# Kernel tuning notes

Measured on AMD Instinct MI355X. Metric: run time of the kernel, lower is better.

## Reference

```python
import jax, jax.numpy as jnp
import numpy as np

B, T, NB, D, E = 2, 4096, 4, 512, 4096
TEMP = 1.0
CAP_F = 1.5
NOISE_KEY = 42


def setup_inputs() -> dict:
    key = jax.random.key(0)
    k1, k2 = jax.random.split(key)
    x = jax.random.normal(k1, (B, T, NB * D), dtype=jnp.float32)
    # Tied weights: embedding_table[i].weight is embedding_decoder[i].weight, shape [E, D] per block
    W = jax.random.normal(k2, (NB, E, D), dtype=jnp.float32) * 0.02
    return {"x": x, "W": W}


def reference(x, W):
    Bv, Tv, _ = x.shape
    xb = x.reshape(Bv, Tv, NB, D)
    expert_capacity = int(Bv * Tv / E * CAP_F)  # = 3 here
    # per-block decoder logits: [B, T, NB, E]
    dist_logits = jnp.einsum('btnd,ned->btne', xb, W)
    # noise = 1 - temperature * rand_like(logits)
    noise = 1.0 - TEMP * jax.random.uniform(jax.random.key(NOISE_KEY), dist_logits.shape, dtype=dist_logits.dtype)
    noisy = dist_logits * noise
    # top-k over the token axis T (dim=1 in torch) per (b, block, element)
    nt = noisy.transpose(0, 2, 3, 1)  # [B, NB, E, T]
    _, topk_idx = jax.lax.top_k(nt, expert_capacity)  # [B, NB, E, k]
    mask = jnp.zeros(nt.shape, dtype=bool)
    bI = jnp.arange(Bv)[:, None, None, None]
    nI = jnp.arange(NB)[None, :, None, None]
    eI = jnp.arange(E)[None, None, :, None]
    mask = mask.at[bI, nI, eI, topk_idx].set(True)
    maskf = mask.transpose(0, 3, 1, 2).astype(noisy.dtype)  # [B, T, NB, E]
    # argmax over codebook dim of masked noisy logits
    decoded_indices = jnp.argmax(maskf * noisy, axis=-1)  # [B, T, NB]
    # embedding gather with tied table W[n]: [B, T, NB, D]
    latents = jax.vmap(lambda w, i: w[i], in_axes=(0, 2), out_axes=2)(W, decoded_indices)
    decoded_latents = latents.reshape(Bv, Tv, NB * D)  # cat along dim=2
    return decoded_indices, decoded_latents, dist_logits
```

## Files before the change

kernel.cpp:

```cpp
#include <hip/hip_runtime.h>
#include <stdint.h>

#define B_     2
#define T_     4096
#define NB_    4
#define D_     512
#define E_     4096
#define NE_    16384
#define HALF_  67108864u
#define SLOTS_ 32768
#define XN8_   2097152
#define WN8_   1048576
#define MT_    32
#define RECN_  (64 * NE_)

typedef unsigned long long u64;
typedef uint32_t u32;
typedef uint16_t u16;
typedef _Float16 f16x8 __attribute__((ext_vector_type(8)));
typedef float    f32x4 __attribute__((ext_vector_type(4)));

#define GLD(srcp, dstp) __builtin_amdgcn_global_load_lds( \
    (const __attribute__((address_space(1))) void*)(srcp), \
    (__attribute__((address_space(3))) void*)(dstp), 16, 0, 0)

__device__ __forceinline__ u32 rotl32(u32 x, int r) { return __builtin_rotateleft32(x, r); }

__device__ __forceinline__ void tf_0_42(u32 x0, u32 x1, u32 &o0, u32 &o1) {
  const u32 ks0 = 0u, ks1 = 42u, ks2 = 0x1BD11BDAu ^ 0u ^ 42u;
  x0 += ks0; x1 += ks1;
#define TFR(r) { x0 += x1; x1 = rotl32(x1, (r)); x1 ^= x0; }
  TFR(13) TFR(15) TFR(26) TFR(6)
  x0 += ks1; x1 += ks2 + 1u;
  TFR(17) TFR(29) TFR(16) TFR(24)
  x0 += ks2; x1 += ks0 + 2u;
  TFR(13) TFR(15) TFR(26) TFR(6)
  x0 += ks0; x1 += ks1 + 3u;
  TFR(17) TFR(29) TFR(16) TFR(24)
  x0 += ks1; x1 += ks2 + 4u;
  TFR(13) TFR(15) TFR(26) TFR(6)
  x0 += ks2; x1 += ks0 + 5u;
#undef TFR
  o0 = x0; o1 = x1;
}

__device__ __forceinline__ float noise_at(u32 i) {
  u32 o0, o1; tf_0_42(0u, i, o0, o1);
  u32 bits = o0 ^ o1;
  float f = __uint_as_float((bits >> 9) | 0x3F800000u);
  return 2.0f - f;
}

__device__ __forceinline__ u32 map_f32(float v) {
  u32 u = __float_as_uint(v);
  u32 s = (u32)((int)u >> 31);
  return u ^ (s | 0x80000000u);
}

__device__ __forceinline__ void merge3(u64 &a0, u64 &a1, u64 &a2,
                                       u64 b0, u64 b1, u64 b2) {
  u64 o0, o1, o2;
  if (a0 >= b0) {
    o0 = a0;
    if (a1 >= b0) { o1 = a1; o2 = (a2 >= b0) ? a2 : b0; }
    else          { o1 = b0; o2 = (a1 >= b1) ? a1 : b1; }
  } else {
    o0 = b0;
    if (b1 >= a0) { o1 = b1; o2 = (b2 >= a0) ? b2 : a0; }
    else          { o1 = a0; o2 = (b1 >= a1) ? b1 : a1; }
  }
  a0 = o0; a1 = o1; a2 = o2;
}

#define BASE_KEY 0x80000000FFFFFFFFull
#define SCALE_   2048.0f
#define INV_SC   (1.0f / 4194304.0f)

__global__ __launch_bounds__(256) void init_keys(u64* __restrict__ keys,
                                                 u32* __restrict__ thr) {
  int i = blockIdx.x * 256 + threadIdx.x;
  keys[i] = BASE_KEY;
  thr[i]  = 0u;
}

__device__ __forceinline__ void split8v(const float4 a0, const float4 a1, f16x8 &hi, f16x8 &lo) {
  float fv[8] = {a0.x, a0.y, a0.z, a0.w, a1.x, a1.y, a1.z, a1.w};
#pragma unroll
  for (int j = 0; j < 8; ++j) {
    float f = fv[j] * SCALE_;
    _Float16 h = (_Float16)f;
    hi[j] = h;
    lo[j] = (_Float16)(f - (float)h);
  }
}

__global__ __launch_bounds__(256) void presplit(const float* __restrict__ x,
                                                const float* __restrict__ W,
                                                f16x8* __restrict__ xh, f16x8* __restrict__ xl,
                                                f16x8* __restrict__ wh, f16x8* __restrict__ wl) {
  size_t g = (size_t)blockIdx.x * 256 + threadIdx.x;
  const float4* src;
  f16x8 *dh, *dl;
  size_t off;
  if (g < XN8_) { src = (const float4*)x; dh = xh; dl = xl; off = g; }
  else          { src = (const float4*)W; dh = wh; dl = wl; off = g - XN8_; }
  float4 a0 = src[off * 2], a1 = src[off * 2 + 1];
  f16x8 hi, lo;
  split8v(a0, a1, hi, lo);
  dh[off] = hi; dl[off] = lo;
}

#define BM 128
#define BN 128

__device__ __forceinline__ void stage_tile(const f16x8* __restrict__ xh,
                                           const f16x8* __restrict__ xl,
                                           const f16x8* __restrict__ wh,
                                           const f16x8* __restrict__ wl,
                                           f16x8* buf, int m0, int n, int e0,
                                           int k0, int w, int lane) {
#pragma unroll
  for (int i = 0; i < 2; ++i) {
    int sbase = w * 128 + i * 64;
    int s  = sbase + lane;
    int r  = s >> 2;
    int ko = (s & 3) ^ ((r >> 1) & 3);
    size_t gA = ((size_t)(m0 + r) * NB_ + n) * (D_ / 8) + k0 + ko;
    size_t gB = ((size_t)n * E_ + e0 + r) * (D_ / 8) + k0 + ko;
    GLD(xh + gA, buf + sbase);
    GLD(xl + gA, buf + 512 + sbase);
    GLD(wh + gB, buf + 1024 + sbase);
    GLD(wl + gB, buf + 1536 + sbase);
  }
}

__device__ __forceinline__ void compute_step(const f16x8* buf, f32x4 acc[4][4],
                                             int wr, int wc, int lm, int lk) {
  const f16x8* Ah = buf;
  const f16x8* Al = buf + 512;
  const f16x8* Bh = buf + 1024;
  const f16x8* Bl = buf + 1536;
  f16x8 bh[4], bl[4];
#pragma unroll
  for (int fn = 0; fn < 4; ++fn) {
    int row = wc * 64 + fn * 16 + lm;
    int ps  = lk ^ ((row >> 1) & 3);
    bh[fn] = Bh[row * 4 + ps];
    bl[fn] = Bl[row * 4 + ps];
  }
#pragma unroll
  for (int fm = 0; fm < 4; ++fm) {
    int row = wr * 64 + fm * 16 + lm;
    int ps  = lk ^ ((row >> 1) & 3);
    f16x8 ah = Ah[row * 4 + ps];
    f16x8 al = Al[row * 4 + ps];
#pragma unroll
    for (int fn = 0; fn < 4; ++fn) {
      acc[fm][fn] = __builtin_amdgcn_mfma_f32_16x16x32_f16(ah, bh[fn], acc[fm][fn], 0, 0, 0);
      acc[fm][fn] = __builtin_amdgcn_mfma_f32_16x16x32_f16(ah, bl[fn], acc[fm][fn], 0, 0, 0);
      acc[fm][fn] = __builtin_amdgcn_mfma_f32_16x16x32_f16(al, bh[fn], acc[fm][fn], 0, 0, 0);
    }
  }
}

__global__ __launch_bounds__(256) void gemm_presample(const f16x8* __restrict__ xh,
                                                      const f16x8* __restrict__ xl,
                                                      const f16x8* __restrict__ wh,
                                                      const f16x8* __restrict__ wl,
                                                      u32* __restrict__ thrbuf) {
  __shared__ f16x8 lds_raw[2048];
  f16x8* AhV = lds_raw;
  f16x8* AlV = lds_raw + 512;
  f16x8* BhV = lds_raw + 1024;
  f16x8* BlV = lds_raw + 1536;

  const int id = blockIdx.x;
  const int e0 = (id & 31) * BN;
  const int n  = (id >> 5) & 3;
  const int b  = id >> 7;

  const int tid  = threadIdx.x;
  const int lane = tid & 63;
  const int wid  = tid >> 6;
  const int wr   = wid >> 1;
  const int wc   = wid & 1;
  const int lm   = lane & 15;
  const int lk   = lane >> 4;

  f32x4 acc[4][4];
#pragma unroll
  for (int i = 0; i < 4; ++i)
#pragma unroll
    for (int j = 0; j < 4; ++j) acc[i][j] = (f32x4){0.f, 0.f, 0.f, 0.f};

  for (int k0 = 0; k0 < D_ / 8; k0 += 4) {
#pragma unroll
    for (int l = 0; l < 2; ++l) {
      int aid = tid + l * 256;
      int r   = aid >> 2;
      int ko  = aid & 3;
      int ps  = ko ^ ((r >> 1) & 3);
      size_t gA = ((size_t)(b * T_ + 32 * r) * NB_ + n) * (D_ / 8) + k0 + ko;
      AhV[r * 4 + ps] = xh[gA];
      AlV[r * 4 + ps] = xl[gA];
      size_t gB = ((size_t)n * E_ + e0 + r) * (D_ / 8) + k0 + ko;
      BhV[r * 4 + ps] = wh[gB];
      BlV[r * 4 + ps] = wl[gB];
    }
    __syncthreads();
    compute_step(lds_raw, acc, wr, wc, lm, lk);
    __syncthreads();
  }
  u64* ldsK = (u64*)lds_raw;

#pragma unroll
  for (int fn = 0; fn < 4; ++fn) {
    const int e  = e0 + wc * 64 + fn * 16 + lm;
    const int ne = n * E_ + e;
    u32 v0 = 0, v1 = 0, v2 = 0;
    u32 tt0 = 0, tt1 = 0, tt2 = 0;
    const u32 ibase = (u32)b * HALF_ + (u32)ne;
#pragma unroll
    for (int fm = 0; fm < 4; ++fm) {
#pragma unroll
      for (int r = 0; r < 4; ++r) {
        const u32 t = 32u * (u32)(wr * 64 + fm * 16 + lk * 4 + r);
        float lg = acc[fm][fn][r] * INV_SC;
        u32 mu = __float_as_uint(fmaxf(lg, 0.0f)) | 0x80000000u;
        if (mu > v2) {
          float y = lg * noise_at(ibase + t * (u32)NE_);
          u32 mv = map_f32(y);
          bool g0 = mv > v0, g1 = mv > v1, g2 = mv > v2;
          v2  = g1 ? v1  : (g2 ? mv : v2);
          tt2 = g1 ? tt1 : (g2 ? t  : tt2);
          v1  = g0 ? v0  : (g1 ? mv : v1);
          tt1 = g0 ? tt0 : (g1 ? t  : tt1);
          v0  = g0 ? mv  : v0;
          tt0 = g0 ? t   : tt0;
        }
      }
    }
    u64 K0 = ((u64)v0 << 32) | (u64)(0xFFFFFFFFu - tt0);
    u64 K1 = ((u64)v1 << 32) | (u64)(0xFFFFFFFFu - tt1);
    u64 K2 = ((u64)v2 << 32) | (u64)(0xFFFFFFFFu - tt2);
    u64 p0 = __shfl_xor(K0, 16), p1 = __shfl_xor(K1, 16), p2 = __shfl_xor(K2, 16);
    merge3(K0, K1, K2, p0, p1, p2);
    p0 = __shfl_xor(K0, 32); p1 = __shfl_xor(K1, 32); p2 = __shfl_xor(K2, 32);
    merge3(K0, K1, K2, p0, p1, p2);
    if (lk == 0) {
      int c = fn * 16 + lm;
      ldsK[(wid * 64 + c) * 3 + 0] = K0;
      ldsK[(wid * 64 + c) * 3 + 1] = K1;
      ldsK[(wid * 64 + c) * 3 + 2] = K2;
    }
  }
  __syncthreads();
  if (wid < 2) {
    int c = lane;
    u64 A0 = ldsK[(wid * 64 + c) * 3 + 0];
    u64 A1 = ldsK[(wid * 64 + c) * 3 + 1];
    u64 A2 = ldsK[(wid * 64 + c) * 3 + 2];
    merge3(A0, A1, A2,
           ldsK[((wid + 2) * 64 + c) * 3 + 0],
           ldsK[((wid + 2) * 64 + c) * 3 + 1],
           ldsK[((wid + 2) * 64 + c) * 3 + 2]);
    int eg = e0 + wid * 64 + c;
    thrbuf[(size_t)b * NE_ + (size_t)n * E_ + eg] = (u32)(A2 >> 32);
  }
}

__global__ __launch_bounds__(256) void gemm_fused(const f16x8* __restrict__ xh,
                                                  const f16x8* __restrict__ xl,
                                                  const f16x8* __restrict__ wh,
                                                  const f16x8* __restrict__ wl,
                                                  float* __restrict__ logits,
                                                  u64* __restrict__ k0g,
                                                  u64* __restrict__ k1g,
                                                  u64* __restrict__ k2g,
                                                  u32* __restrict__ thrbuf) {
  __shared__ f16x8 lds_raw[4096];
  f16x8* bufA = lds_raw;
  f16x8* bufB = lds_raw + 2048;

  const int id = blockIdx.x;
  const int e0 = (id & 31) * BN;
  const int mt = (id >> 5) & 63;
  const int n  = id >> 11;
  const int m0 = mt * BM;

  const int tid  = threadIdx.x;
  const int lane = tid & 63;
  const int wid  = tid >> 6;
  const int wr   = wid >> 1;
  const int wc   = wid & 1;
  const int lm   = lane & 15;
  const int lk   = lane >> 4;

  f32x4 acc[4][4];
#pragma unroll
  for (int i = 0; i < 4; ++i)
#pragma unroll
    for (int j = 0; j < 4; ++j) acc[i][j] = (f32x4){0.f, 0.f, 0.f, 0.f};

  stage_tile(xh, xl, wh, wl, bufA, m0, n, e0, 0, wid, lane);
  __syncthreads();
  for (int kk = 0; kk < 16; kk += 2) {
    stage_tile(xh, xl, wh, wl, bufB, m0, n, e0, 4 * (kk + 1), wid, lane);
    compute_step(bufA, acc, wr, wc, lm, lk);
    __syncthreads();
    if (kk < 14)
      stage_tile(xh, xl, wh, wl, bufA, m0, n, e0, 4 * (kk + 2), wid, lane);
    compute_step(bufB, acc, wr, wc, lm, lk);
    __syncthreads();
  }

  float* lgbuf = (float*)lds_raw;
  u16*   tbuf  = (u16*)((char*)lds_raw + 16384);
  u64*   ldsK  = (u64*)((char*)lds_raw + 24576);

  const int b     = m0 >> 12;
  const int mbase = m0 & (T_ - 1);
  const int mtile = mbase >> 7;

#pragma unroll
  for (int fm = 0; fm < 4; ++fm) {
#pragma unroll
    for (int r = 0; r < 4; ++r) {
      int m = m0 + wr * 64 + fm * 16 + lk * 4 + r;
      float* row = logits + ((size_t)m * NB_ + n) * E_ + e0 + wc * 64 + lm;
#pragma unroll
      for (int fn = 0; fn < 4; ++fn)
        __builtin_nontemporal_store(acc[fm][fn][r] * INV_SC, row + fn * 16);
    }
  }

#pragma unroll
  for (int fn = 0; fn < 4; ++fn) {
    const int e  = e0 + wc * 64 + fn * 16 + lm;
    const int ne = n * E_ + e;
    const u32 thrv = thrbuf[(size_t)b * NE_ + ne];

    int cnt = 0;
#pragma unroll
    for (int fm = 0; fm < 4; ++fm) {
#pragma unroll
      for (int r = 0; r < 4; ++r) {
        float lg = acc[fm][fn][r] * INV_SC;
        u32 mu = __float_as_uint(fmaxf(lg, 0.0f)) | 0x80000000u;
        if (mu >= thrv) {
          lgbuf[cnt * 256 + tid] = lg;
          tbuf [cnt * 256 + tid] = (u16)(mbase + wr * 64 + fm * 16 + lk * 4 + r);
          ++cnt;
        }
      }
    }

    u32 v0 = 0, v1 = 0, v2 = 0;
    u32 tt0 = 0, tt1 = 0, tt2 = 0;
    const u32 ibase = (u32)b * HALF_ + (u32)ne;
    for (int k = 0; k < cnt; ++k) {
      float lg = lgbuf[k * 256 + tid];
      u32 t    = (u32)tbuf[k * 256 + tid];
      float y  = lg * noise_at(ibase + t * (u32)NE_);
      u32 mv = map_f32(y);
      bool g0 = mv > v0, g1 = mv > v1, g2 = mv > v2;
      v2  = g1 ? v1  : (g2 ? mv : v2);
      tt2 = g1 ? tt1 : (g2 ? t  : tt2);
      v1  = g0 ? v0  : (g1 ? mv : v1);
      tt1 = g0 ? tt0 : (g1 ? t  : tt1);
      v0  = g0 ? mv  : v0;
      tt0 = g0 ? t   : tt0;
    }

    u64 K0 = ((u64)v0 << 32) | (u64)(0xFFFFFFFFu - tt0);
    u64 K1 = ((u64)v1 << 32) | (u64)(0xFFFFFFFFu - tt1);
    u64 K2 = ((u64)v2 << 32) | (u64)(0xFFFFFFFFu - tt2);
    u64 p0 = __shfl_xor(K0, 16), p1 = __shfl_xor(K1, 16), p2 = __shfl_xor(K2, 16);
    merge3(K0, K1, K2, p0, p1, p2);
    p0 = __shfl_xor(K0, 32); p1 = __shfl_xor(K1, 32); p2 = __shfl_xor(K2, 32);
    merge3(K0, K1, K2, p0, p1, p2);
    if (lk == 0) {
      int c = fn * 16 + lm;
      ldsK[(wid * 64 + c) * 3 + 0] = K0;
      ldsK[(wid * 64 + c) * 3 + 1] = K1;
      ldsK[(wid * 64 + c) * 3 + 2] = K2;
    }
  }
  __syncthreads();
  if (wid < 2) {
    int c = lane;
    u64 A0 = ldsK[(wid * 64 + c) * 3 + 0];
    u64 A1 = ldsK[(wid * 64 + c) * 3 + 1];
    u64 A2 = ldsK[(wid * 64 + c) * 3 + 2];
    u64 C0 = ldsK[((wid + 2) * 64 + c) * 3 + 0];
    u64 C1 = ldsK[((wid + 2) * 64 + c) * 3 + 1];
    u64 C2 = ldsK[((wid + 2) * 64 + c) * 3 + 2];
    merge3(A0, A1, A2, C0, C1, C2);
    int eg = e0 + wid * 64 + c;
    size_t R = (size_t)(mtile * 2 + b) * NE_ + (size_t)n * E_ + eg;
    __builtin_nontemporal_store(A0, k0g + R);
    __builtin_nontemporal_store(A1, k1g + R);
    __builtin_nontemporal_store(A2, k2g + R);
    atomicMax(&thrbuf[(size_t)b * NE_ + (size_t)n * E_ + eg], (u32)(A2 >> 32));
  }
}

__global__ __launch_bounds__(256) void merge_scatter2(const u64* __restrict__ k0g,
                                                      const u64* __restrict__ k1g,
                                                      const u64* __restrict__ k2g,
                                                      u64* __restrict__ keys) {
  int gid2 = blockIdx.x * 256 + threadIdx.x;
  int b  = gid2 >> 14;
  int ne = gid2 & (NE_ - 1);

  u64 K0 = 0, K1 = 0, K2 = 0;
  for (int mt = 0; mt < MT_; ++mt) {
    size_t R = (size_t)(mt * 2 + b) * NE_ + ne;
    merge3(K0, K1, K2, k0g[R], k1g[R], k2g[R]);
  }

  int n = ne >> 12;
  u32 e = (u32)(ne & (E_ - 1));
  u64 elo = (u64)(0xFFFFFFFFu - e);
  u32 t0 = 0xFFFFFFFFu - (u32)K0;
  u32 t1 = 0xFFFFFFFFu - (u32)K1;
  u32 t2 = 0xFFFFFFFFu - (u32)K2;
  atomicMax(&keys[((size_t)b * T_ + t0) * NB_ + n], (K0 & 0xFFFFFFFF00000000ull) | elo);
  atomicMax(&keys[((size_t)b * T_ + t1) * NB_ + n], (K1 & 0xFFFFFFFF00000000ull) | elo);
  atomicMax(&keys[((size_t)b * T_ + t2) * NB_ + n], (K2 & 0xFFFFFFFF00000000ull) | elo);
}

__device__ __forceinline__ void split8(const float* __restrict__ p, f16x8 &hi, f16x8 &lo) {
  float4 a0 = *(const float4*)p;
  float4 a1 = *(const float4*)(p + 4);
  split8v(a0, a1, hi, lo);
}

__global__ __launch_bounds__(256) void gemm_logits_fb(const float* __restrict__ x,
                                                      const float* __restrict__ W,
                                                      float* __restrict__ logits) {
  __shared__ f16x8 lds_raw[2048];
  f16x8* AhV = lds_raw;
  f16x8* AlV = lds_raw + 512;
  f16x8* BhV = lds_raw + 1024;
  f16x8* BlV = lds_raw + 1536;

  const int n  = blockIdx.z;
  const int m0 = blockIdx.y * BM;
  const int e0 = blockIdx.x * BN;
  const int tid  = threadIdx.x;
  const int lane = tid & 63;
  const int wid  = tid >> 6;
  const int wr   = wid >> 1;
  const int wc   = wid & 1;
  const int lm   = lane & 15;
  const int lk   = lane >> 4;

  const float* Abase = x + ((size_t)m0 * NB_ + n) * D_;
  const float* Bbase = W + ((size_t)n * E_ + e0) * D_;

  f32x4 acc[4][4];
#pragma unroll
  for (int i = 0; i < 4; ++i)
#pragma unroll
    for (int j = 0; j < 4; ++j) acc[i][j] = (f32x4){0.f, 0.f, 0.f, 0.f};

  for (int k0 = 0; k0 < D_; k0 += 32) {
#pragma unroll
    for (int l = 0; l < 2; ++l) {
      int aid = tid + l * 256;
      int r   = aid >> 2;
      int ko  = aid & 3;
      int ps  = ko ^ ((r >> 1) & 3);
      f16x8 hi, lo;
      split8(Abase + (size_t)r * (NB_ * D_) + k0 + ko * 8, hi, lo);
      AhV[r * 4 + ps] = hi; AlV[r * 4 + ps] = lo;
      split8(Bbase + (size_t)r * D_ + k0 + ko * 8, hi, lo);
      BhV[r * 4 + ps] = hi; BlV[r * 4 + ps] = lo;
    }
    __syncthreads();
    compute_step(lds_raw, acc, wr, wc, lm, lk);
    __syncthreads();
  }

#pragma unroll
  for (int fm = 0; fm < 4; ++fm) {
#pragma unroll
    for (int fn = 0; fn < 4; ++fn) {
#pragma unroll
      for (int r = 0; r < 4; ++r) {
        int m = m0 + wr * 64 + fm * 16 + lk * 4 + r;
        int e = e0 + wc * 64 + fn * 16 + lm;
        logits[((size_t)m * NB_ + n) * E_ + e] = acc[fm][fn][r] * INV_SC;
      }
    }
  }
}

__global__ __launch_bounds__(256) void select_scatter(const float* __restrict__ logits,
                                                      u64* __restrict__ keys) {
  int gid = blockIdx.x * 256 + threadIdx.x;
  int b  = gid >> 14;
  int ne = gid & (NE_ - 1);

  float v0 = -1e30f, v1 = -1e30f, v2 = -1e30f;
  int   t0 = 0, t1 = 0, t2 = 0;

  const float* lg = logits + (size_t)b * HALF_;
  const u32 ib = (u32)b * HALF_ + (u32)ne;
  for (int t = 0; t < T_; ++t) {
    u32 i0 = (u32)t * (u32)NE_ + (u32)ne;
    float y = lg[i0] * noise_at(ib + (u32)t * (u32)NE_);
    if (y > v0)      { v2=v1; t2=t1; v1=v0; t1=t0; v0=y; t0=t; }
    else if (y > v1) { v2=v1; t2=t1; v1=y;  t1=t; }
    else if (y > v2) { v2=y;  t2=t; }
  }

  int n = ne >> 12;
  int e = ne & (E_ - 1);
  u64 klo = 0xFFFFFFFFull - (u32)e;
  atomicMax(&keys[((size_t)b * T_ + t0) * NB_ + n], ((u64)map_f32(v0) << 32) | klo);
  atomicMax(&keys[((size_t)b * T_ + t1) * NB_ + n], ((u64)map_f32(v1) << 32) | klo);
  atomicMax(&keys[((size_t)b * T_ + t2) * NB_ + n], ((u64)map_f32(v2) << 32) | klo);
}

__global__ __launch_bounds__(128) void finalize(const u64* __restrict__ keys,
                                                const float* __restrict__ W,
                                                float* __restrict__ out_idx,
                                                float* __restrict__ out_lat) {
  int slot = blockIdx.x;
  int n = slot & (NB_ - 1);
  int e = (int)(0xFFFFFFFFu - (u32)keys[slot]) & (E_ - 1);
  if (threadIdx.x == 0) out_idx[slot] = (float)e;

  const float4 v = ((const float4*)(W + ((size_t)n * E_ + e) * D_))[threadIdx.x];
  ((float4*)(out_lat + (size_t)slot * D_))[threadIdx.x] = v;
}

extern "C" void kernel_launch(void* const* d_in, const int* in_sizes, int n_in,
                              void* d_out, int out_size, void* d_ws, size_t ws_size,
                              hipStream_t stream) {
  const float* x = (const float*)d_in[0];
  const float* W = (const float*)d_in[1];

  float* out_idx    = (float*)d_out;
  float* out_lat    = out_idx + (size_t)SLOTS_;
  float* out_logits = out_lat + (size_t)SLOTS_ * D_;

  u64* keys = (u64*)d_ws;
  const size_t KEYS_B = (size_t)SLOTS_ * 8;
  const size_t THR_B  = (size_t)SLOTS_ * 4;
  const size_t XH_B   = (size_t)XN8_ * 16;
  const size_t WH_B   = (size_t)WN8_ * 16;
  bool split = ws_size >= KEYS_B + THR_B + 2 * XH_B + 2 * WH_B;

  u32*   thr = (u32*)((char*)d_ws + KEYS_B);
  char*  sp  = (char*)d_ws + KEYS_B + THR_B;
  f16x8* xh  = (f16x8*)sp;
  f16x8* xl  = (f16x8*)(sp + XH_B);
  f16x8* wh  = (f16x8*)(sp + 2 * XH_B);
  f16x8* wl  = (f16x8*)(sp + 2 * XH_B + WH_B);

  u64* k0g = (u64*)out_lat;
  u64* k1g = k0g + RECN_;
  u64* k2g = k1g + RECN_;

  init_keys<<<SLOTS_ / 256, 256, 0, stream>>>(keys, thr);

  if (split) {
    presplit<<<(XN8_ + WN8_) / 256, 256, 0, stream>>>(x, W, xh, xl, wh, wl);
    gemm_presample<<<256, 256, 0, stream>>>(xh, xl, wh, wl, thr);
    gemm_fused<<<8192, 256, 0, stream>>>(xh, xl, wh, wl, out_logits, k0g, k1g, k2g, thr);
    merge_scatter2<<<SLOTS_ / 256, 256, 0, stream>>>(k0g, k1g, k2g, keys);
  } else {
    dim3 ggrid(E_ / BN, (B_ * T_) / BM, NB_);
    gemm_logits_fb<<<ggrid, 256, 0, stream>>>(x, W, out_logits);
    select_scatter<<<SLOTS_ / 256, 256, 0, stream>>>(out_logits, keys);
  }

  finalize<<<SLOTS_, 128, 0, stream>>>(keys, W, out_idx, out_lat);
}
```

Baseline: 611.5 us.

## Use 8 waves per block in fused GEMM with 64x32 warp tiles

The fused GEMM+top-k kernel now launches 512 threads (8 waves) per block instead of 256, arranged 2x4, so each wave computes a 64x32 sub-tile with half the accumulators. Staging is spread over all 8 waves with one load per thread per buffer, and the epilogue scratch buffers, LDS offsets and the cross-wave merge are re-indexed for 8 waves. The intent is more waves in flight to hide latency and lower register pressure, at the cost of more per-wave redundant A-fragment LDS reads and more threads taking part in each synchronisation.

```diff
diff --git a/kernel.cpp b/kernel.cpp
--- a/kernel.cpp
+++ b/kernel.cpp
@@ -113,27 +113,6 @@
 #define BM 128
 #define BN 128
 
-__device__ __forceinline__ void stage_tile(const f16x8* __restrict__ xh,
-                                           const f16x8* __restrict__ xl,
-                                           const f16x8* __restrict__ wh,
-                                           const f16x8* __restrict__ wl,
-                                           f16x8* buf, int m0, int n, int e0,
-                                           int k0, int w, int lane) {
-#pragma unroll
-  for (int i = 0; i < 2; ++i) {
-    int sbase = w * 128 + i * 64;
-    int s  = sbase + lane;
-    int r  = s >> 2;
-    int ko = (s & 3) ^ ((r >> 1) & 3);
-    size_t gA = ((size_t)(m0 + r) * NB_ + n) * (D_ / 8) + k0 + ko;
-    size_t gB = ((size_t)n * E_ + e0 + r) * (D_ / 8) + k0 + ko;
-    GLD(xh + gA, buf + sbase);
-    GLD(xl + gA, buf + 512 + sbase);
-    GLD(wh + gB, buf + 1024 + sbase);
-    GLD(wl + gB, buf + 1536 + sbase);
-  }
-}
-
 __device__ __forceinline__ void compute_step(const f16x8* buf, f32x4 acc[4][4],
                                              int wr, int wc, int lm, int lk) {
   const f16x8* Ah = buf;
@@ -156,6 +135,53 @@
     f16x8 al = Al[row * 4 + ps];
 #pragma unroll
     for (int fn = 0; fn < 4; ++fn) {
+      acc[fm][fn] = __builtin_amdgcn_mfma_f32_16x16x32_f16(ah, bh[fn], acc[fm][fn], 0, 0, 0);
+      acc[fm][fn] = __builtin_amdgcn_mfma_f32_16x16x32_f16(ah, bl[fn], acc[fm][fn], 0, 0, 0);
+      acc[fm][fn] = __builtin_amdgcn_mfma_f32_16x16x32_f16(al, bh[fn], acc[fm][fn], 0, 0, 0);
+    }
+  }
+}
+
+__device__ __forceinline__ void stage_tile8(const f16x8* __restrict__ xh,
+                                            const f16x8* __restrict__ xl,
+                                            const f16x8* __restrict__ wh,
+                                            const f16x8* __restrict__ wl,
+                                            f16x8* buf, int m0, int n, int e0,
+                                            int k0, int w, int lane) {
+  int sbase = w * 64;
+  int s  = sbase + lane;
+  int r  = s >> 2;
+  int ko = (s & 3) ^ ((r >> 1) & 3);
+  size_t gA = ((size_t)(m0 + r) * NB_ + n) * (D_ / 8) + k0 + ko;
+  size_t gB = ((size_t)n * E_ + e0 + r) * (D_ / 8) + k0 + ko;
+  GLD(xh + gA, buf + sbase);
+  GLD(xl + gA, buf + 512 + sbase);
+  GLD(wh + gB, buf + 1024 + sbase);
+  GLD(wl + gB, buf + 1536 + sbase);
+}
+
+__device__ __forceinline__ void compute_step8(const f16x8* buf, f32x4 acc[4][2],
+                                              int wr, int wc, int lm, int lk) {
+  const f16x8* Ah = buf;
+  const f16x8* Al = buf + 512;
+  const f16x8* Bh = buf + 1024;
+  const f16x8* Bl = buf + 1536;
+  f16x8 bh[2], bl[2];
+#pragma unroll
+  for (int fn = 0; fn < 2; ++fn) {
+    int row = wc * 32 + fn * 16 + lm;
+    int ps  = lk ^ ((row >> 1) & 3);
+    bh[fn] = Bh[row * 4 + ps];
+    bl[fn] = Bl[row * 4 + ps];
+  }
+#pragma unroll
+  for (int fm = 0; fm < 4; ++fm) {
+    int row = wr * 64 + fm * 16 + lm;
+    int ps  = lk ^ ((row >> 1) & 3);
+    f16x8 ah = Ah[row * 4 + ps];
+    f16x8 al = Al[row * 4 + ps];
+#pragma unroll
+    for (int fn = 0; fn < 2; ++fn) {
       acc[fm][fn] = __builtin_amdgcn_mfma_f32_16x16x32_f16(ah, bh[fn], acc[fm][fn], 0, 0, 0);
       acc[fm][fn] = __builtin_amdgcn_mfma_f32_16x16x32_f16(ah, bl[fn], acc[fm][fn], 0, 0, 0);
       acc[fm][fn] = __builtin_amdgcn_mfma_f32_16x16x32_f16(al, bh[fn], acc[fm][fn], 0, 0, 0);
@@ -269,15 +295,15 @@
   }
 }
 
-__global__ __launch_bounds__(256) void gemm_fused(const f16x8* __restrict__ xh,
-                                                  const f16x8* __restrict__ xl,
-                                                  const f16x8* __restrict__ wh,
-                                                  const f16x8* __restrict__ wl,
-                                                  float* __restrict__ logits,
-                                                  u64* __restrict__ k0g,
-                                                  u64* __restrict__ k1g,
-                                                  u64* __restrict__ k2g,
-                                                  u32* __restrict__ thrbuf) {
+__global__ __launch_bounds__(512, 4) void gemm_fused(const f16x8* __restrict__ xh,
+                                                     const f16x8* __restrict__ xl,
+                                                     const f16x8* __restrict__ wh,
+                                                     const f16x8* __restrict__ wl,
+                                                     float* __restrict__ logits,
+                                                     u64* __restrict__ k0g,
+                                                     u64* __restrict__ k1g,
+                                                     u64* __restrict__ k2g,
+                                                     u32* __restrict__ thrbuf) {
   __shared__ f16x8 lds_raw[4096];
   f16x8* bufA = lds_raw;
   f16x8* bufB = lds_raw + 2048;
@@ -291,32 +317,32 @@
   const int tid  = threadIdx.x;
   const int lane = tid & 63;
   const int wid  = tid >> 6;
-  const int wr   = wid >> 1;
-  const int wc   = wid & 1;
+  const int wr   = wid >> 2;
+  const int wc   = wid & 3;
   const int lm   = lane & 15;
   const int lk   = lane >> 4;
 
-  f32x4 acc[4][4];
+  f32x4 acc[4][2];
 #pragma unroll
   for (int i = 0; i < 4; ++i)
 #pragma unroll
-    for (int j = 0; j < 4; ++j) acc[i][j] = (f32x4){0.f, 0.f, 0.f, 0.f};
-
-  stage_tile(xh, xl, wh, wl, bufA, m0, n, e0, 0, wid, lane);
+    for (int j = 0; j < 2; ++j) acc[i][j] = (f32x4){0.f, 0.f, 0.f, 0.f};
+
+  stage_tile8(xh, xl, wh, wl, bufA, m0, n, e0, 0, wid, lane);
   __syncthreads();
   for (int kk = 0; kk < 16; kk += 2) {
-    stage_tile(xh, xl, wh, wl, bufB, m0, n, e0, 4 * (kk + 1), wid, lane);
-    compute_step(bufA, acc, wr, wc, lm, lk);
+    stage_tile8(xh, xl, wh, wl, bufB, m0, n, e0, 4 * (kk + 1), wid, lane);
+    compute_step8(bufA, acc, wr, wc, lm, lk);
     __syncthreads();
     if (kk < 14)
-      stage_tile(xh, xl, wh, wl, bufA, m0, n, e0, 4 * (kk + 2), wid, lane);
-    compute_step(bufB, acc, wr, wc, lm, lk);
+      stage_tile8(xh, xl, wh, wl, bufA, m0, n, e0, 4 * (kk + 2), wid, lane);
+    compute_step8(bufB, acc, wr, wc, lm, lk);
     __syncthreads();
   }
 
   float* lgbuf = (float*)lds_raw;
-  u16*   tbuf  = (u16*)((char*)lds_raw + 16384);
-  u64*   ldsK  = (u64*)((char*)lds_raw + 24576);
+  u16*   tbuf  = (u16*)((char*)lds_raw + 32768);
+  u64*   ldsK  = (u64*)((char*)lds_raw + 49152);
 
   const int b     = m0 >> 12;
   const int mbase = m0 & (T_ - 1);
@@ -327,16 +353,16 @@
 #pragma unroll
     for (int r = 0; r < 4; ++r) {
       int m = m0 + wr * 64 + fm * 16 + lk * 4 + r;
-      float* row = logits + ((size_t)m * NB_ + n) * E_ + e0 + wc * 64 + lm;
-#pragma unroll
-      for (int fn = 0; fn < 4; ++fn)
+      float* row = logits + ((size_t)m * NB_ + n) * E_ + e0 + wc * 32 + lm;
+#pragma unroll
+      for (int fn = 0; fn < 2; ++fn)
         __builtin_nontemporal_store(acc[fm][fn][r] * INV_SC, row + fn * 16);
     }
   }
 
 #pragma unroll
-  for (int fn = 0; fn < 4; ++fn) {
-    const int e  = e0 + wc * 64 + fn * 16 + lm;
+  for (int fn = 0; fn < 2; ++fn) {
+    const int e  = e0 + wc * 32 + fn * 16 + lm;
     const int ne = n * E_ + e;
     const u32 thrv = thrbuf[(size_t)b * NE_ + ne];
 
@@ -348,8 +374,8 @@
         float lg = acc[fm][fn][r] * INV_SC;
         u32 mu = __float_as_uint(fmaxf(lg, 0.0f)) | 0x80000000u;
         if (mu >= thrv) {
-          lgbuf[cnt * 256 + tid] = lg;
-          tbuf [cnt * 256 + tid] = (u16)(mbase + wr * 64 + fm * 16 + lk * 4 + r);
+          lgbuf[cnt * 512 + tid] = lg;
+          tbuf [cnt * 512 + tid] = (u16)(mbase + wr * 64 + fm * 16 + lk * 4 + r);
           ++cnt;
         }
       }
@@ -359,8 +385,8 @@
     u32 tt0 = 0, tt1 = 0, tt2 = 0;
     const u32 ibase = (u32)b * HALF_ + (u32)ne;
     for (int k = 0; k < cnt; ++k) {
-      float lg = lgbuf[k * 256 + tid];
-      u32 t    = (u32)tbuf[k * 256 + tid];
+      float lg = lgbuf[k * 512 + tid];
+      u32 t    = (u32)tbuf[k * 512 + tid];
       float y  = lg * noise_at(ibase + t * (u32)NE_);
       u32 mv = map_f32(y);
       bool g0 = mv > v0, g1 = mv > v1, g2 = mv > v2;
@@ -381,22 +407,22 @@
     merge3(K0, K1, K2, p0, p1, p2);
     if (lk == 0) {
       int c = fn * 16 + lm;
-      ldsK[(wid * 64 + c) * 3 + 0] = K0;
-      ldsK[(wid * 64 + c) * 3 + 1] = K1;
-      ldsK[(wid * 64 + c) * 3 + 2] = K2;
+      ldsK[(wid * 32 + c) * 3 + 0] = K0;
+      ldsK[(wid * 32 + c) * 3 + 1] = K1;
+      ldsK[(wid * 32 + c) * 3 + 2] = K2;
     }
   }
   __syncthreads();
-  if (wid < 2) {
+  if (wid < 4 && lane < 32) {
     int c = lane;
-    u64 A0 = ldsK[(wid * 64 + c) * 3 + 0];
-    u64 A1 = ldsK[(wid * 64 + c) * 3 + 1];
-    u64 A2 = ldsK[(wid * 64 + c) * 3 + 2];
-    u64 C0 = ldsK[((wid + 2) * 64 + c) * 3 + 0];
-    u64 C1 = ldsK[((wid + 2) * 64 + c) * 3 + 1];
-    u64 C2 = ldsK[((wid + 2) * 64 + c) * 3 + 2];
+    u64 A0 = ldsK[(wid * 32 + c) * 3 + 0];
+    u64 A1 = ldsK[(wid * 32 + c) * 3 + 1];
+    u64 A2 = ldsK[(wid * 32 + c) * 3 + 2];
+    u64 C0 = ldsK[((wid + 4) * 32 + c) * 3 + 0];
+    u64 C1 = ldsK[((wid + 4) * 32 + c) * 3 + 1];
+    u64 C2 = ldsK[((wid + 4) * 32 + c) * 3 + 2];
     merge3(A0, A1, A2, C0, C1, C2);
-    int eg = e0 + wid * 64 + c;
+    int eg = e0 + wid * 32 + c;
     size_t R = (size_t)(mtile * 2 + b) * NE_ + (size_t)n * E_ + eg;
     __builtin_nontemporal_store(A0, k0g + R);
     __builtin_nontemporal_store(A1, k1g + R);
@@ -570,7 +596,7 @@
   if (split) {
     presplit<<<(XN8_ + WN8_) / 256, 256, 0, stream>>>(x, W, xh, xl, wh, wl);
     gemm_presample<<<256, 256, 0, stream>>>(xh, xl, wh, wl, thr);
-    gemm_fused<<<8192, 256, 0, stream>>>(xh, xl, wh, wl, out_logits, k0g, k1g, k2g, thr);
+    gemm_fused<<<8192, 512, 0, stream>>>(xh, xl, wh, wl, out_logits, k0g, k1g, k2g, thr);
     merge_scatter2<<<SLOTS_ / 256, 256, 0, stream>>>(k0g, k1g, k2g, keys);
   } else {
     dim3 ggrid(E_ / BN, (B_ * T_) / BM, NB_);
```

New measurement: 579.8 us. 5.2% less time.
